# Kernel optimization log

Measured on AMD Instinct MI355X. Metric: run time of the kernel, lower is better.

The kernel has to match this reference:

```python
import jax, jax.numpy as jnp
import numpy as np

N_RECTS = 200000
GRID = 256


def setup_inputs() -> dict:
    key = jax.random.key(0)
    k1, k2, k3 = jax.random.split(key, 3)
    # unit placement region [0,1] x [0,1]
    boundary = jnp.array([[0.0, 0.0], [1.0, 1.0]], dtype=jnp.float32)
    # lower-left corners in [0, 1); cell sizes ~ a few bins wide (bin = 1/GRID)
    xy = jax.random.uniform(k1, (N_RECTS, 2), dtype=jnp.float32)
    dims = jax.random.uniform(k2, (N_RECTS, 2), dtype=jnp.float32) * (3.0 / GRID)
    charge_weight = jax.random.uniform(k3, (N_RECTS,), dtype=jnp.float32) + 0.5
    return {"boundary": boundary, "xy": xy, "dims": dims,
            "charge_weight": charge_weight, "grid_size": GRID}


def reference(boundary, xy, dims, charge_weight, grid_size):
    G = grid_size
    dtype = xy.dtype
    xmin, ymin = boundary[0, 0], boundary[0, 1]
    xmax, ymax = boundary[1, 0], boundary[1, 1]
    lx = (xmax - xmin) / G
    ly = (ymax - ymin) / G
    idx = jnp.arange(G, dtype=dtype)
    gx0 = xmin + idx * lx   # [G] bin left edges
    gy0 = ymin + idx * ly
    gx1 = gx0 + lx
    gy1 = gy0 + ly
    bx0 = xy[:, 0]
    by0 = xy[:, 1]
    bx1 = bx0 + dims[:, 0]
    by1 = by0 + dims[:, 1]
    # per-rect / per-bin 1D overlaps: [N, G]
    ox = jnp.maximum(jnp.minimum(gx1[None, :], bx1[:, None]) -
                     jnp.maximum(gx0[None, :], bx0[:, None]), 0.0)
    oy = jnp.maximum(jnp.minimum(gy1[None, :], by1[:, None]) -
                     jnp.maximum(gy0[None, :], by0[:, None]), 0.0)
    # sum over chunks of weighted outer products == one big matmul:
    # field[i, j] = sum_n w[n] * ox[n, i] * oy[n, j]
    field = jnp.einsum('ni,nj->ij', ox * charge_weight[:, None], oy)
    return field / (lx * ly)
```

## Files before the change

### kernel.cpp

```cpp
#include <hip/hip_runtime.h>
#include <math.h>

__global__ __launch_bounds__(1024)
void strip_scan(const float* __restrict__ boundary,
                const float2* __restrict__ xy,
                const float2* __restrict__ dims,
                const float* __restrict__ w,
                float* __restrict__ ws,
                int G, int R, int rows, int n_rects)
{
    extern __shared__ float acc[];
    const int b   = blockIdx.x;
    const int s   = b / R;
    const int r   = b % R;
    const int tid = threadIdx.x;
    const int stripElems = rows * G;
    const int row0 = s * rows;
    const int row1 = row0 + rows - 1;

    for (int c = tid; c < stripElems; c += blockDim.x) acc[c] = 0.0f;
    __syncthreads();

    const float xmin = boundary[0], ymin = boundary[1];
    const float xmax = boundary[2], ymax = boundary[3];
    const float lx = (xmax - xmin) / (float)G;
    const float ly = (ymax - ymin) / (float)G;
    const float inv_lx = (float)G / (xmax - xmin);
    const float inv_ly = (float)G / (ymax - ymin);
    const float inv_area = inv_lx * inv_ly;

    const int chunk = (n_rects + R - 1) / R;
    const int lo = r * chunk;
    const int hi = min(lo + chunk, n_rects);

    for (int n = lo + tid; n < hi; n += blockDim.x) {
        float2 p = xy[n];
        float2 d = dims[n];
        const float bx0 = p.x, bx1 = p.x + d.x;

        int i0 = (int)floorf((bx0 - xmin) * inv_lx);
        int i1 = (int)floorf((bx1 - xmin) * inv_lx);
        i0 = max(max(i0, 0), row0);
        i1 = min(min(i1, G - 1), row1);
        if (i0 > i1) continue;

        const float by0 = p.y, by1 = p.y + d.y;
        int j0 = max((int)floorf((by0 - ymin) * inv_ly), 0);
        int j1 = min((int)floorf((by1 - ymin) * inv_ly), G - 1);
        if (j0 > j1) continue;

        const float cw = w[n] * inv_area;

        for (int i = i0; i <= i1; ++i) {
            float gx0 = xmin + (float)i * lx;
            float ox  = fminf(gx0 + lx, bx1) - fmaxf(gx0, bx0);
            if (ox <= 0.0f) continue;
            float cox = cw * ox;
            float* rowp = acc + (i - row0) * G;
            for (int j = j0; j <= j1; ++j) {
                float gy0 = ymin + (float)j * ly;
                float oy  = fminf(gy0 + ly, by1) - fmaxf(gy0, by0);
                if (oy > 0.0f)
                    atomicAdd(rowp + j, cox * oy);
            }
        }
    }
    __syncthreads();

    float* dst = ws + (size_t)b * stripElems;
    for (int c = tid; c < stripElems; c += blockDim.x) dst[c] = acc[c];
}

__global__ __launch_bounds__(256)
void reduce_strips(const float* __restrict__ ws,
                   float* __restrict__ out,
                   int G, int R, int rows)
{
    const int c = blockIdx.x * blockDim.x + threadIdx.x;
    if (c >= G * G) return;
    const int i = c / G;
    const int j = c - i * G;
    const int s = i / rows;
    const int stripElems = rows * G;
    const int local = (i - s * rows) * G + j;

    const float* base = ws + (size_t)s * R * stripElems + local;
    float sum = 0.0f;
    #pragma unroll 8
    for (int r = 0; r < R; ++r)
        sum += base[(size_t)r * stripElems];
    out[c] = sum;
}

__global__ void scatter_direct(const float* __restrict__ boundary,
                               const float2* __restrict__ xy,
                               const float2* __restrict__ dims,
                               const float* __restrict__ w,
                               float* __restrict__ out,
                               int G, int n_rects)
{
    int n = blockIdx.x * blockDim.x + threadIdx.x;
    if (n >= n_rects) return;
    float xmin = boundary[0], ymin = boundary[1];
    float xmax = boundary[2], ymax = boundary[3];
    float lx = (xmax - xmin) / (float)G;
    float ly = (ymax - ymin) / (float)G;
    float2 p = xy[n]; float2 d = dims[n];
    float bx0 = p.x, by0 = p.y, bx1 = bx0 + d.x, by1 = by0 + d.y;
    float cw = w[n] / (lx * ly);
    int i0 = max((int)floorf((bx0 - xmin) / lx), 0);
    int i1 = min((int)floorf((bx1 - xmin) / lx), G - 1);
    int j0 = max((int)floorf((by0 - ymin) / ly), 0);
    int j1 = min((int)floorf((by1 - ymin) / ly), G - 1);
    for (int i = i0; i <= i1; ++i) {
        float gx0 = xmin + (float)i * lx;
        float ox = fmaxf(fminf(gx0 + lx, bx1) - fmaxf(gx0, bx0), 0.0f);
        if (ox <= 0.0f) continue;
        float cox = cw * ox;
        for (int j = j0; j <= j1; ++j) {
            float gy0 = ymin + (float)j * ly;
            float oy = fmaxf(fminf(gy0 + ly, by1) - fmaxf(gy0, by0), 0.0f);
            if (oy > 0.0f) atomicAdd(out + (size_t)i * G + j, cox * oy);
        }
    }
}

extern "C" void kernel_launch(void* const* d_in, const int* in_sizes, int n_in,
                              void* d_out, int out_size, void* d_ws, size_t ws_size,
                              hipStream_t stream) {
    const float*  boundary = (const float*)d_in[0];
    const float2* xy       = (const float2*)d_in[1];
    const float2* dims     = (const float2*)d_in[2];
    const float*  cweight  = (const float*)d_in[3];
    float* out = (float*)d_out;
    const int n_rects = in_sizes[1] / 2;

    int G = (int)lround(sqrt((double)out_size));
    const bool square = ((long long)G * G == (long long)out_size) && G > 0;

    int S = 0, rows = 0;
    if (square) {
        for (int cand = 1; cand <= 64; cand <<= 1) {
            if (G % cand) continue;
            long long bytes = (long long)(G / cand) * G * 4;
            if (bytes <= 64 * 1024) { S = cand; rows = G / cand; break; }
        }
    }
    int R = 0;
    if (S > 0) {
        R = 256 / S;
        if (R < 1) R = 1;
        long long need = (long long)S * R * rows * G * 4;
        while (R > 1 && need > (long long)ws_size) {
            R >>= 1;
            need = (long long)S * R * rows * G * 4;
        }
        if (need > (long long)ws_size) R = 0;
    }

    if (R > 0) {
        float* ws = (float*)d_ws;
        const int stripBytes = rows * G * 4;
        strip_scan<<<S * R, 1024, stripBytes, stream>>>(
            boundary, xy, dims, cweight, ws, G, R, rows, n_rects);
        reduce_strips<<<(G * G + 255) / 256, 256, 0, stream>>>(
            ws, out, G, R, rows);
    } else {
        hipMemsetAsync(out, 0, (size_t)out_size * sizeof(float), stream);
        const int block = 256;
        scatter_direct<<<(n_rects + block - 1) / block, block, 0, stream>>>(
            boundary, xy, dims, cweight, out, G, n_rects);
    }
}
```

Baseline: 82.87 us.

## Shrink strip LDS to 32KB, double blocks, unroll small-rect scatter path

Strips are now capped at 32KB of LDS instead of 64KB, so G=256 gets 8 strips of 32 rows, and the block count doubles via R=512/S. A min-blocks-per-SM hint of 2 is added to the launch bounds. Rectangles covering at most 4x4 bins take a fully unrolled branch that computes the overlaps once and issues predicated atomics. The aim is more resident blocks and less loop overhead, at the price of every block scanning more rectangles, a larger workspace and a longer reduction.

```diff
diff --git a/kernel.cpp b/kernel.cpp
--- a/kernel.cpp
+++ b/kernel.cpp
@@ -1,7 +1,7 @@
 #include <hip/hip_runtime.h>
 #include <math.h>
 
-__global__ __launch_bounds__(1024)
+__global__ __launch_bounds__(1024, 2)
 void strip_scan(const float* __restrict__ boundary,
                 const float2* __restrict__ xy,
                 const float2* __restrict__ dims,
@@ -38,10 +38,10 @@
         float2 d = dims[n];
         const float bx0 = p.x, bx1 = p.x + d.x;
 
-        int i0 = (int)floorf((bx0 - xmin) * inv_lx);
-        int i1 = (int)floorf((bx1 - xmin) * inv_lx);
-        i0 = max(max(i0, 0), row0);
-        i1 = min(min(i1, G - 1), row1);
+        int ri0 = (int)floorf((bx0 - xmin) * inv_lx);
+        int ri1 = (int)floorf((bx1 - xmin) * inv_lx);
+        int i0 = max(max(ri0, 0), row0);
+        int i1 = min(min(ri1, G - 1), row1);
         if (i0 > i1) continue;
 
         const float by0 = p.y, by1 = p.y + d.y;
@@ -51,17 +51,46 @@
 
         const float cw = w[n] * inv_area;
 
-        for (int i = i0; i <= i1; ++i) {
-            float gx0 = xmin + (float)i * lx;
-            float ox  = fminf(gx0 + lx, bx1) - fmaxf(gx0, bx0);
-            if (ox <= 0.0f) continue;
-            float cox = cw * ox;
-            float* rowp = acc + (i - row0) * G;
-            for (int j = j0; j <= j1; ++j) {
+        if (i1 - i0 <= 3 && j1 - j0 <= 3) {
+            float oxv[4], oyv[4];
+            #pragma unroll
+            for (int di = 0; di < 4; ++di) {
+                int   i   = i0 + di;
+                float gx0 = xmin + (float)i * lx;
+                float ox  = fminf(gx0 + lx, bx1) - fmaxf(gx0, bx0);
+                oxv[di] = (i <= i1) ? fmaxf(ox, 0.0f) : 0.0f;
+            }
+            #pragma unroll
+            for (int dj = 0; dj < 4; ++dj) {
+                int   j   = j0 + dj;
                 float gy0 = ymin + (float)j * ly;
                 float oy  = fminf(gy0 + ly, by1) - fmaxf(gy0, by0);
-                if (oy > 0.0f)
-                    atomicAdd(rowp + j, cox * oy);
+                oyv[dj] = (j <= j1) ? fmaxf(oy, 0.0f) : 0.0f;
+            }
+            #pragma unroll
+            for (int di = 0; di < 4; ++di) {
+                if (oxv[di] > 0.0f) {
+                    float  cox  = cw * oxv[di];
+                    float* rowp = acc + (i0 + di - row0) * G + j0;
+                    #pragma unroll
+                    for (int dj = 0; dj < 4; ++dj) {
+                        if (oyv[dj] > 0.0f)
+                            atomicAdd(rowp + dj, cox * oyv[dj]);
+                    }
+                }
+            }
+        } else {
+            for (int i = i0; i <= i1; ++i) {
+                float gx0 = xmin + (float)i * lx;
+                float ox  = fmaxf(fminf(gx0 + lx, bx1) - fmaxf(gx0, bx0), 0.0f);
+                if (ox <= 0.0f) continue;
+                float cox = cw * ox;
+                float* rowp = acc + (i - row0) * G;
+                for (int j = j0; j <= j1; ++j) {
+                    float gy0 = ymin + (float)j * ly;
+                    float oy  = fminf(gy0 + ly, by1) - fmaxf(gy0, by0);
+                    if (oy > 0.0f) atomicAdd(rowp + j, cox * oy);
+                }
             }
         }
     }
@@ -140,15 +169,22 @@
 
     int S = 0, rows = 0;
     if (square) {
-        for (int cand = 1; cand <= 64; cand <<= 1) {
+        for (int cand = 1; cand <= 256; cand <<= 1) {
             if (G % cand) continue;
             long long bytes = (long long)(G / cand) * G * 4;
-            if (bytes <= 64 * 1024) { S = cand; rows = G / cand; break; }
+            if (bytes <= 32 * 1024) { S = cand; rows = G / cand; break; }
+        }
+        if (S == 0) {
+            for (int cand = 1; cand <= 256; cand <<= 1) {
+                if (G % cand) continue;
+                long long bytes = (long long)(G / cand) * G * 4;
+                if (bytes <= 64 * 1024) { S = cand; rows = G / cand; break; }
+            }
         }
     }
     int R = 0;
     if (S > 0) {
-        R = 256 / S;
+        R = 512 / S;
         if (R < 1) R = 1;
         long long need = (long long)S * R * rows * G * 4;
         while (R > 1 && need > (long long)ws_size) {
```

Result: no change. 84.34 us (+1.8%).
